# Performance work log

Measured on AMD Instinct MI355X. Metric: run time of the kernel, lower is better.

## Reference

```python
import jax, jax.numpy as jnp
import numpy as np

# ---- static configuration (matches init_kwargs / input_specs) ----
B, N = 4, 128            # images, proposals per image
C = 256                  # feature channels (in_channels)
HF, WF = 23, 30          # feature map size (input 736x960 / 32)
PH, PW = 7, 7            # pooled_size
SCALE = 1.0 / 32.0       # scale_factor
HIMG, WIMG = HF * 32, WF * 32
KH = HF // PH + 2        # max rows any pooling bin can span
KW = WF // PW + 2        # max cols any pooling bin can span
HID, OUT = 256, 5
NEG = -1e30


def _roi_pool_one(f, box):
    """Quantized ROI max pooling for one proposal.
    f: (C, HF, WF) feature map; box: (4,) [x1,y1,x2,y2] in feature coords.
    Returns (C, PH, PW)."""
    box = jax.lax.stop_gradient(box)  # indices are non-differentiable
    x1 = jnp.clip(jnp.floor(box[0]).astype(jnp.int32), 0, WF - 1)
    y1 = jnp.clip(jnp.floor(box[1]).astype(jnp.int32), 0, HF - 1)
    roi_w = jnp.clip(jnp.ceil(box[2]).astype(jnp.int32) - x1, 1, WF)
    roi_h = jnp.clip(jnp.ceil(box[3]).astype(jnp.int32) - y1, 1, HF)
    ph = jnp.arange(PH)
    pw = jnp.arange(PW)
    hs = y1 + (ph * roi_h) // PH                       # bin row starts (PH,)
    he = y1 + ((ph + 1) * roi_h + PH - 1) // PH        # bin row ends (ceil)
    ws = x1 + (pw * roi_w) // PW
    we = x1 + ((pw + 1) * roi_w + PW - 1) // PW
    hidx = hs[:, None] + jnp.arange(KH)[None, :]       # (PH, KH)
    hval = (hidx < he[:, None]) & (hidx < HF)
    widx = ws[:, None] + jnp.arange(KW)[None, :]       # (PW, KW)
    wval = (widx < we[:, None]) & (widx < WF)
    rows = f[:, jnp.clip(hidx, 0, HF - 1), :]          # (C, PH, KH, WF) gather
    rmax = jnp.max(jnp.where(hval[None, :, :, None], rows, NEG), axis=2)  # (C, PH, WF)
    cols = rmax[:, :, jnp.clip(widx, 0, WF - 1)]       # (C, PH, PW, KW) gather
    return jnp.max(jnp.where(wval[None, None], cols, NEG), axis=3)        # (C, PH, PW)


# vmap over proposals, then over images: (B,C,HF,WF),(B,N,4) -> (B,N,C,PH,PW)
_roi_pool = jax.vmap(jax.vmap(_roi_pool_one, in_axes=(None, 0)), in_axes=(0, 0))


def setup_inputs() -> dict:
    key = jax.random.key(0)
    ks = jax.random.split(key, 8)
    features = jax.random.normal(ks[0], (B, C, HF, WF), jnp.float32)
    # valid proposals in image coordinates (min box side ~32 px)
    x1 = jax.random.uniform(ks[1], (B, N)) * (WIMG - 32.0)
    y1 = jax.random.uniform(ks[2], (B, N)) * (HIMG - 32.0)
    x2 = x1 + 32.0 + jax.random.uniform(ks[3], (B, N)) * (WIMG - 32.0 - x1)
    y2 = y1 + 32.0 + jax.random.uniform(ks[4], (B, N)) * (HIMG - 32.0 - y1)
    conf = jax.random.normal(ks[5], (B, N))
    proposals = jnp.stack([x1, y1, x2, y2, conf], axis=-1)  # (B, N, 5)
    W1 = jax.random.normal(ks[6], (HID, C * PH * PW), jnp.float32) * 0.01
    b1 = jnp.zeros((HID,), jnp.float32)
    W2 = jax.random.normal(ks[7], (OUT, HID), jnp.float32) * 0.01
    b2 = jnp.zeros((OUT,), jnp.float32)
    return {"features": features, "proposals": proposals,
            "W1": W1, "b1": b1, "W2": W2, "b2": b2}


def reference(features, proposals, W1, b1, W2, b2):
    boxes_feat = proposals[..., :4] * SCALE                 # image -> feature coords
    pooled = _roi_pool(features, boxes_feat)                # (B, N, C, PH, PW)
    flat = pooled.reshape(B, N, C * PH * PW)
    h = jax.nn.relu(jnp.einsum('bnf,hf->bnh', flat, W1) + b1)
    out = jnp.einsum('bnh,oh->bno', h, W2) + b2             # (B, N, 5)
    refined_boxes = proposals[..., :4] + out[..., :4]
    refined_conf = jax.nn.sigmoid(proposals[..., 4:5] + out[..., 4:5])
    return jnp.concatenate([refined_boxes, refined_conf], axis=-1)  # (B, N, 5)
```

## Files before the change

kernel.cpp:

```cpp
#include <hip/hip_runtime.h>
#include <math.h>

#define Bq 4
#define Nq 128
#define Cq 256
#define HFq 23
#define WFq 30
#define PHq 7
#define PWq 7
#define HIDq 256
#define OUTq 5
#define Fq (Cq*PHq*PWq)
#define Mq (Bq*Nq)
#define HWq (HFq*WFq)
#define SCALEq (1.0f/32.0f)
#define NEGq (-1e30f)
#define KHq 5
#define KWq 6
#define SPLITK 14
#define KCH (Fq/SPLITK)
#define KSTEPS (KCH/32)

typedef float f32x4 __attribute__((ext_vector_type(4)));
typedef __bf16 bf16x8 __attribute__((ext_vector_type(8)));

__device__ __forceinline__ unsigned short f2b(float f) {
    unsigned int u = __float_as_uint(f);
    unsigned int r = (u + 0x7FFFu + ((u >> 16) & 1u)) >> 16;
    return (unsigned short)r;
}

__global__ __launch_bounds__(256) void k_prep(const float* __restrict__ feat,
                                              float* __restrict__ ft,
                                              const float* __restrict__ W1,
                                              unsigned short* __restrict__ w1p,
                                              float* __restrict__ h) {
    __shared__ __align__(16) unsigned short smem[Fq];
    int bid = blockIdx.x;
    int tid = threadIdx.x;
    if (bid < 704) {
        float (*t)[33] = (float (*)[33])smem;
        int bb  = bid / 176;
        int rem = bid % 176;
        int x0 = (rem % 22) * 32;
        int c0 = (rem / 22) * 32;
        int tx = tid & 31, ty = tid >> 5;
        const float* src = feat + (size_t)bb * Cq * HWq;
        float* dst = ft + (size_t)bb * HWq * Cq;
#pragma unroll
        for (int i = 0; i < 4; ++i) {
            int c = c0 + ty + i * 8;
            int x = x0 + tx;
            if (x < HWq) t[ty + i * 8][tx] = src[(size_t)c * HWq + x];
        }
        __syncthreads();
#pragma unroll
        for (int i = 0; i < 4; ++i) {
            int x = x0 + ty + i * 8;
            int c = c0 + tx;
            if (x < HWq) dst[(size_t)x * Cq + c] = t[tx][ty + i * 8];
        }
    } else if (bid < 960) {
        int j = bid - 704;
        const float4* src = (const float4*)(W1 + (size_t)j * Fq);
        for (int i = tid; i < Fq / 4; i += 256) {
            float4 v = src[i];
            ushort4 o;
            o.x = f2b(v.x); o.y = f2b(v.y); o.z = f2b(v.z); o.w = f2b(v.w);
            ((ushort4*)smem)[i] = o;
        }
        __syncthreads();
        uint4* dst = (uint4*)(w1p + (size_t)j * Fq);
        for (int i = tid; i < Fq / 8; i += 256) {
            int base = i * 8;
            int cell = base >> 8;
            int c0v = base & 255;
            unsigned short tmp[8];
#pragma unroll
            for (int u = 0; u < 8; ++u) tmp[u] = smem[(c0v + u) * 49 + cell];
            dst[i] = *(const uint4*)tmp;
        }
    } else {
        f32x4* h4 = (f32x4*)h;
        int base = (bid - 960) * 4096;
        f32x4 z = {0.f, 0.f, 0.f, 0.f};
#pragma unroll
        for (int u = 0; u < 16; ++u) h4[base + u * 256 + tid] = z;
    }
}

__global__ __launch_bounds__(256) void k_pool(const float* __restrict__ ft,
                                              const float* __restrict__ props,
                                              unsigned short* __restrict__ pooled) {
    int wave = threadIdx.x >> 6;
    int lane = threadIdx.x & 63;
    int g = blockIdx.y * 4 + wave;
    int m = blockIdx.x;
    int b = m >> 7;
    const float* pr = props + (size_t)m * 5;
    float b0 = pr[0] * SCALEq, b1v = pr[1] * SCALEq;
    float b2v = pr[2] * SCALEq, b3v = pr[3] * SCALEq;
    int x1 = min(max((int)floorf(b0), 0), WFq - 1);
    int y1 = min(max((int)floorf(b1v), 0), HFq - 1);
    int rw = min(max((int)ceilf(b2v) - x1, 1), WFq);
    int rh = min(max((int)ceilf(b3v) - y1, 1), HFq);
    const float* ftb = ft + (size_t)b * HWq * Cq + lane * 4;
    unsigned short* pm = pooled + (size_t)m * Fq + lane * 4;

    for (int cell = g; cell < PHq * PWq; cell += 8) {
        int ph = cell / 7;
        int pw = cell - ph * 7;
        int hs = y1 + (ph * rh) / PHq;
        int he = min(y1 + ((ph + 1) * rh + PHq - 1) / PHq, HFq);
        int ws = x1 + (pw * rw) / PWq;
        int we = min(x1 + ((pw + 1) * rw + PWq - 1) / PWq, WFq);
        f32x4 acc = {NEGq, NEGq, NEGq, NEGq};
#pragma unroll
        for (int kh = 0; kh < KHq; ++kh) {
            if (hs + kh < he) {
                const float* rowp = ftb + (size_t)((hs + kh) * WFq) * Cq;
#pragma unroll
                for (int kw = 0; kw < KWq; ++kw) {
                    if (ws + kw < we) {
                        f32x4 v = *(const f32x4*)(rowp + (size_t)(ws + kw) * Cq);
                        acc.x = fmaxf(acc.x, v.x);
                        acc.y = fmaxf(acc.y, v.y);
                        acc.z = fmaxf(acc.z, v.z);
                        acc.w = fmaxf(acc.w, v.w);
                    }
                }
            }
        }
        ushort4 o;
        o.x = f2b(acc.x); o.y = f2b(acc.y); o.z = f2b(acc.z); o.w = f2b(acc.w);
        *(ushort4*)(pm + (size_t)cell * Cq) = o;
    }
}

__global__ __launch_bounds__(256) void k_gemm1(const unsigned short* __restrict__ pooled,
                                               const unsigned short* __restrict__ w1p,
                                               float* __restrict__ h) {
    __shared__ __align__(16) unsigned short As[64 * 32];
    __shared__ __align__(16) unsigned short Bs[64 * 32];
    int m0 = blockIdx.x * 64;
    int j0 = blockIdx.y * 64;
    int kz = blockIdx.z;
    int tid = threadIdx.x;
    int r = tid >> 2, qq = tid & 3;
    const uint4* ap = (const uint4*)(pooled + (size_t)(m0 + r) * Fq + (size_t)kz * KCH + qq * 8);
    const uint4* bp = (const uint4*)(w1p + (size_t)(j0 + r) * Fq + (size_t)kz * KCH + qq * 8);
    int lane = tid & 63, wv = tid >> 6;
    int q = lane >> 4, mr = lane & 15;
    f32x4 acc0 = {0.f, 0.f, 0.f, 0.f};
    f32x4 acc1 = {0.f, 0.f, 0.f, 0.f};
    f32x4 acc2 = {0.f, 0.f, 0.f, 0.f};
    f32x4 acc3 = {0.f, 0.f, 0.f, 0.f};
    const bf16x8* afp = (const bf16x8*)(As + (wv * 16 + mr) * 32 + q * 8);
    const bf16x8* bfp0 = (const bf16x8*)(Bs + (0 + mr) * 32 + q * 8);
    const bf16x8* bfp1 = (const bf16x8*)(Bs + (16 + mr) * 32 + q * 8);
    const bf16x8* bfp2 = (const bf16x8*)(Bs + (32 + mr) * 32 + q * 8);
    const bf16x8* bfp3 = (const bf16x8*)(Bs + (48 + mr) * 32 + q * 8);
    uint4* asw = (uint4*)(As + r * 32 + qq * 8);
    uint4* bsw = (uint4*)(Bs + r * 32 + qq * 8);
    uint4 av = ap[0];
    uint4 bv = bp[0];
    for (int s = 0; s < KSTEPS; ++s) {
        __syncthreads();
        *asw = av;
        *bsw = bv;
        __syncthreads();
        if (s + 1 < KSTEPS) {
            av = ap[(s + 1) * 4];
            bv = bp[(s + 1) * 4];
        }
        bf16x8 a = *afp;
        acc0 = __builtin_amdgcn_mfma_f32_16x16x32_bf16(a, *bfp0, acc0, 0, 0, 0);
        acc1 = __builtin_amdgcn_mfma_f32_16x16x32_bf16(a, *bfp1, acc1, 0, 0, 0);
        acc2 = __builtin_amdgcn_mfma_f32_16x16x32_bf16(a, *bfp2, acc2, 0, 0, 0);
        acc3 = __builtin_amdgcn_mfma_f32_16x16x32_bf16(a, *bfp3, acc3, 0, 0, 0);
    }
    int mb = m0 + wv * 16 + q * 4;
    int jj = j0 + mr;
#pragma unroll
    for (int r2 = 0; r2 < 4; ++r2) {
        float* row = h + (size_t)(mb + r2) * HIDq + jj;
        atomicAdd(row + 0,  acc0[r2]);
        atomicAdd(row + 16, acc1[r2]);
        atomicAdd(row + 32, acc2[r2]);
        atomicAdd(row + 48, acc3[r2]);
    }
}

__global__ __launch_bounds__(256) void k_tail(const float* __restrict__ h,
                                              const float* __restrict__ b1,
                                              const float* __restrict__ W2,
                                              const float* __restrict__ b2,
                                              const float* __restrict__ props,
                                              float* __restrict__ out) {
    __shared__ float red[OUTq][4];
    int m = blockIdx.x, j = threadIdx.x;
    float hv = fmaxf(h[(size_t)m * HIDq + j] + b1[j], 0.f);
    float p[OUTq];
#pragma unroll
    for (int o = 0; o < OUTq; ++o) p[o] = hv * W2[(size_t)o * HIDq + j];
    int lane = j & 63, wid = j >> 6;
#pragma unroll
    for (int o = 0; o < OUTq; ++o) {
        float v = p[o];
        v += __shfl_xor(v, 1);
        v += __shfl_xor(v, 2);
        v += __shfl_xor(v, 4);
        v += __shfl_xor(v, 8);
        v += __shfl_xor(v, 16);
        v += __shfl_xor(v, 32);
        if (lane == 0) red[o][wid] = v;
    }
    __syncthreads();
    if (j < OUTq) {
        float s = red[j][0] + red[j][1] + red[j][2] + red[j][3] + b2[j];
        float pv = props[(size_t)m * 5 + j];
        float r;
        if (j < 4) r = pv + s;
        else r = 1.f / (1.f + expf(-(pv + s)));
        out[(size_t)m * 5 + j] = r;
    }
}

extern "C" void kernel_launch(void* const* d_in, const int* in_sizes, int n_in,
                              void* d_out, int out_size, void* d_ws, size_t ws_size,
                              hipStream_t stream) {
    const float* feat  = (const float*)d_in[0];
    const float* props = (const float*)d_in[1];
    const float* W1    = (const float*)d_in[2];
    const float* b1    = (const float*)d_in[3];
    const float* W2    = (const float*)d_in[4];
    const float* b2    = (const float*)d_in[5];
    float* out = (float*)d_out;

    char* ws = (char*)d_ws;
    float* ft              = (float*)(ws);
    unsigned short* w1p    = (unsigned short*)(ws + 2826240);
    unsigned short* pooled = (unsigned short*)(ws + 9248768);
    float* h               = (float*)(ws + 22093824);

    k_prep<<<968, 256, 0, stream>>>(feat, ft, W1, w1p, h);
    k_pool<<<dim3(Mq, 2), 256, 0, stream>>>(ft, props, pooled);
    k_gemm1<<<dim3(8, 4, SPLITK), 256, 0, stream>>>(pooled, w1p, h);
    k_tail<<<Mq, 256, 0, stream>>>(h, b1, W2, b2, props, out);
}
```

Baseline: 126.5 us.

## Store transposed features as bf16, widen pooling loads, double-buffer GEMM LDS

The prep kernel now writes the channel-last feature copy in bf16 instead of fp32, which halves that buffer and the traffic of the pooling gathers. The pooling kernel loads 8 bf16 channels per lane, splits each bin's columns between the two half-waves, and merges them with a cross-lane shuffle. The split-K GEMM switches to double-buffered shared-memory tiles, removing one barrier per k-step and prefetching two steps ahead. Max-pooling on bf16 inputs gives the same values as pooling in fp32 and rounding afterwards, so accuracy is unchanged, but the workspace offsets had to be repacked.

```diff
diff --git a/kernel.cpp b/kernel.cpp
--- a/kernel.cpp
+++ b/kernel.cpp
@@ -23,6 +23,7 @@
 
 typedef float f32x4 __attribute__((ext_vector_type(4)));
 typedef __bf16 bf16x8 __attribute__((ext_vector_type(8)));
+typedef unsigned short u16x8 __attribute__((ext_vector_type(8)));
 
 __device__ __forceinline__ unsigned short f2b(float f) {
     unsigned int u = __float_as_uint(f);
@@ -31,7 +32,7 @@
 }
 
 __global__ __launch_bounds__(256) void k_prep(const float* __restrict__ feat,
-                                              float* __restrict__ ft,
+                                              unsigned short* __restrict__ ft,
                                               const float* __restrict__ W1,
                                               unsigned short* __restrict__ w1p,
                                               float* __restrict__ h) {
@@ -46,7 +47,7 @@
         int c0 = (rem / 22) * 32;
         int tx = tid & 31, ty = tid >> 5;
         const float* src = feat + (size_t)bb * Cq * HWq;
-        float* dst = ft + (size_t)bb * HWq * Cq;
+        unsigned short* dst = ft + (size_t)bb * HWq * Cq;
 #pragma unroll
         for (int i = 0; i < 4; ++i) {
             int c = c0 + ty + i * 8;
@@ -54,11 +55,17 @@
             if (x < HWq) t[ty + i * 8][tx] = src[(size_t)c * HWq + x];
         }
         __syncthreads();
-#pragma unroll
-        for (int i = 0; i < 4; ++i) {
-            int x = x0 + ty + i * 8;
-            int c = c0 + tx;
-            if (x < HWq) dst[(size_t)x * Cq + c] = t[tx][ty + i * 8];
+        int u = tid & 15, xl = tid >> 4;
+#pragma unroll
+        for (int i = 0; i < 2; ++i) {
+            int xloc = xl + i * 16;
+            int x = x0 + xloc;
+            if (x < HWq) {
+                ushort2 o;
+                o.x = f2b(t[u * 2][xloc]);
+                o.y = f2b(t[u * 2 + 1][xloc]);
+                *(ushort2*)(dst + (size_t)x * Cq + c0 + u * 2) = o;
+            }
         }
     } else if (bid < 960) {
         int j = bid - 704;
@@ -77,7 +84,7 @@
             int c0v = base & 255;
             unsigned short tmp[8];
 #pragma unroll
-            for (int u = 0; u < 8; ++u) tmp[u] = smem[(c0v + u) * 49 + cell];
+            for (int u2 = 0; u2 < 8; ++u2) tmp[u2] = smem[(c0v + u2) * 49 + cell];
             dst[i] = *(const uint4*)tmp;
         }
     } else {
@@ -85,15 +92,17 @@
         int base = (bid - 960) * 4096;
         f32x4 z = {0.f, 0.f, 0.f, 0.f};
 #pragma unroll
-        for (int u = 0; u < 16; ++u) h4[base + u * 256 + tid] = z;
-    }
-}
-
-__global__ __launch_bounds__(256) void k_pool(const float* __restrict__ ft,
+        for (int u2 = 0; u2 < 16; ++u2) h4[base + u2 * 256 + tid] = z;
+    }
+}
+
+__global__ __launch_bounds__(256) void k_pool(const unsigned short* __restrict__ ft,
                                               const float* __restrict__ props,
                                               unsigned short* __restrict__ pooled) {
     int wave = threadIdx.x >> 6;
     int lane = threadIdx.x & 63;
+    int half = lane >> 5;
+    int cl = lane & 31;
     int g = blockIdx.y * 4 + wave;
     int m = blockIdx.x;
     int b = m >> 7;
@@ -104,8 +113,8 @@
     int y1 = min(max((int)floorf(b1v), 0), HFq - 1);
     int rw = min(max((int)ceilf(b2v) - x1, 1), WFq);
     int rh = min(max((int)ceilf(b3v) - y1, 1), HFq);
-    const float* ftb = ft + (size_t)b * HWq * Cq + lane * 4;
-    unsigned short* pm = pooled + (size_t)m * Fq + lane * 4;
+    const unsigned short* ftb = ft + (size_t)b * HWq * Cq + cl * 8;
+    unsigned short* pm = pooled + (size_t)m * Fq + cl * 8;
 
     for (int cell = g; cell < PHq * PWq; cell += 8) {
         int ph = cell / 7;
@@ -114,34 +123,41 @@
         int he = min(y1 + ((ph + 1) * rh + PHq - 1) / PHq, HFq);
         int ws = x1 + (pw * rw) / PWq;
         int we = min(x1 + ((pw + 1) * rw + PWq - 1) / PWq, WFq);
-        f32x4 acc = {NEGq, NEGq, NEGq, NEGq};
+        float acc[8];
+#pragma unroll
+        for (int u = 0; u < 8; ++u) acc[u] = NEGq;
 #pragma unroll
         for (int kh = 0; kh < KHq; ++kh) {
             if (hs + kh < he) {
-                const float* rowp = ftb + (size_t)((hs + kh) * WFq) * Cq;
-#pragma unroll
-                for (int kw = 0; kw < KWq; ++kw) {
-                    if (ws + kw < we) {
-                        f32x4 v = *(const f32x4*)(rowp + (size_t)(ws + kw) * Cq);
-                        acc.x = fmaxf(acc.x, v.x);
-                        acc.y = fmaxf(acc.y, v.y);
-                        acc.z = fmaxf(acc.z, v.z);
-                        acc.w = fmaxf(acc.w, v.w);
+                const unsigned short* rowp = ftb + (size_t)((hs + kh) * WFq) * Cq;
+#pragma unroll
+                for (int kw2 = 0; kw2 < 3; ++kw2) {
+                    int w = ws + kw2 * 2 + half;
+                    if (w < we) {
+                        u16x8 v = *(const u16x8*)(rowp + (size_t)w * Cq);
+#pragma unroll
+                        for (int u = 0; u < 8; ++u)
+                            acc[u] = fmaxf(acc[u], __uint_as_float((unsigned)v[u] << 16));
                     }
                 }
             }
         }
-        ushort4 o;
-        o.x = f2b(acc.x); o.y = f2b(acc.y); o.z = f2b(acc.z); o.w = f2b(acc.w);
-        *(ushort4*)(pm + (size_t)cell * Cq) = o;
+#pragma unroll
+        for (int u = 0; u < 8; ++u) acc[u] = fmaxf(acc[u], __shfl_xor(acc[u], 32));
+        if (half == 0) {
+            u16x8 o;
+#pragma unroll
+            for (int u = 0; u < 8; ++u) o[u] = f2b(acc[u]);
+            *(u16x8*)(pm + (size_t)cell * Cq) = o;
+        }
     }
 }
 
 __global__ __launch_bounds__(256) void k_gemm1(const unsigned short* __restrict__ pooled,
                                                const unsigned short* __restrict__ w1p,
                                                float* __restrict__ h) {
-    __shared__ __align__(16) unsigned short As[64 * 32];
-    __shared__ __align__(16) unsigned short Bs[64 * 32];
+    __shared__ __align__(16) unsigned short As[2][64 * 32];
+    __shared__ __align__(16) unsigned short Bs[2][64 * 32];
     int m0 = blockIdx.x * 64;
     int j0 = blockIdx.y * 64;
     int kz = blockIdx.z;
@@ -155,29 +171,33 @@
     f32x4 acc1 = {0.f, 0.f, 0.f, 0.f};
     f32x4 acc2 = {0.f, 0.f, 0.f, 0.f};
     f32x4 acc3 = {0.f, 0.f, 0.f, 0.f};
-    const bf16x8* afp = (const bf16x8*)(As + (wv * 16 + mr) * 32 + q * 8);
-    const bf16x8* bfp0 = (const bf16x8*)(Bs + (0 + mr) * 32 + q * 8);
-    const bf16x8* bfp1 = (const bf16x8*)(Bs + (16 + mr) * 32 + q * 8);
-    const bf16x8* bfp2 = (const bf16x8*)(Bs + (32 + mr) * 32 + q * 8);
-    const bf16x8* bfp3 = (const bf16x8*)(Bs + (48 + mr) * 32 + q * 8);
-    uint4* asw = (uint4*)(As + r * 32 + qq * 8);
-    uint4* bsw = (uint4*)(Bs + r * 32 + qq * 8);
+    int stoff = r * 32 + qq * 8;
+    int aoff = (wv * 16 + mr) * 32 + q * 8;
+    int boff = mr * 32 + q * 8;
+
     uint4 av = ap[0];
     uint4 bv = bp[0];
+    *(uint4*)(As[0] + stoff) = av;
+    *(uint4*)(Bs[0] + stoff) = bv;
+    av = ap[4];
+    bv = bp[4];
+#pragma unroll 2
     for (int s = 0; s < KSTEPS; ++s) {
         __syncthreads();
-        *asw = av;
-        *bsw = bv;
-        __syncthreads();
+        int cur = s & 1;
         if (s + 1 < KSTEPS) {
-            av = ap[(s + 1) * 4];
-            bv = bp[(s + 1) * 4];
-        }
-        bf16x8 a = *afp;
-        acc0 = __builtin_amdgcn_mfma_f32_16x16x32_bf16(a, *bfp0, acc0, 0, 0, 0);
-        acc1 = __builtin_amdgcn_mfma_f32_16x16x32_bf16(a, *bfp1, acc1, 0, 0, 0);
-        acc2 = __builtin_amdgcn_mfma_f32_16x16x32_bf16(a, *bfp2, acc2, 0, 0, 0);
-        acc3 = __builtin_amdgcn_mfma_f32_16x16x32_bf16(a, *bfp3, acc3, 0, 0, 0);
+            *(uint4*)(As[cur ^ 1] + stoff) = av;
+            *(uint4*)(Bs[cur ^ 1] + stoff) = bv;
+            if (s + 2 < KSTEPS) {
+                av = ap[(s + 2) * 4];
+                bv = bp[(s + 2) * 4];
+            }
+        }
+        bf16x8 a = *(const bf16x8*)(As[cur] + aoff);
+        acc0 = __builtin_amdgcn_mfma_f32_16x16x32_bf16(a, *(const bf16x8*)(Bs[cur] + boff),            acc0, 0, 0, 0);
+        acc1 = __builtin_amdgcn_mfma_f32_16x16x32_bf16(a, *(const bf16x8*)(Bs[cur] + boff + 16 * 32), acc1, 0, 0, 0);
+        acc2 = __builtin_amdgcn_mfma_f32_16x16x32_bf16(a, *(const bf16x8*)(Bs[cur] + boff + 32 * 32), acc2, 0, 0, 0);
+        acc3 = __builtin_amdgcn_mfma_f32_16x16x32_bf16(a, *(const bf16x8*)(Bs[cur] + boff + 48 * 32), acc3, 0, 0, 0);
     }
     int mb = m0 + wv * 16 + q * 4;
     int jj = j0 + mr;
@@ -238,10 +258,10 @@
     float* out = (float*)d_out;
 
     char* ws = (char*)d_ws;
-    float* ft              = (float*)(ws);
-    unsigned short* w1p    = (unsigned short*)(ws + 2826240);
-    unsigned short* pooled = (unsigned short*)(ws + 9248768);
-    float* h               = (float*)(ws + 22093824);
+    unsigned short* ft     = (unsigned short*)(ws);
+    unsigned short* w1p    = (unsigned short*)(ws + 1413120);
+    unsigned short* pooled = (unsigned short*)(ws + 7835648);
+    float* h               = (float*)(ws + 20680704);
 
     k_prep<<<968, 256, 0, stream>>>(feat, ft, W1, w1p, h);
     k_pool<<<dim3(Mq, 2), 256, 0, stream>>>(ft, props, pooled);
```

Result: faster. 120.8 us (-4.5%).
